# Kernel tuning notes

Hardware: AMD Instinct MI355X
Metric: run time of the kernel (lower is better)

The kernel has to match this reference:

```python
import jax, jax.numpy as jnp
import numpy as np

N_NODES = 50000
N_EDGES = 800000
IN_DIM = 128
HID_DIM = 128


def gcn_conv(x, edge_index, W, b):
    # PyG GCNConv: out = D^{-1/2} (A + I) D^{-1/2} X W + b
    n = x.shape[0]
    loop = jnp.arange(n)
    src = jnp.concatenate([edge_index[0], loop])
    dst = jnp.concatenate([edge_index[1], loop])
    deg = jax.ops.segment_sum(jnp.ones_like(dst, dtype=x.dtype), dst, num_segments=n)
    dinv = jax.lax.rsqrt(jnp.maximum(deg, 1.0))  # deg >= 1 with self-loops
    norm = dinv[src] * dinv[dst]                 # [E+N]
    h = x @ W                                    # [N, out_dim] dense transform first (smaller msgs)
    msg = h[src] * norm[:, None]                 # gather + scale
    return jax.ops.segment_sum(msg, dst, num_segments=n) + b  # scatter-add


def gcn_backbone(x, edge_index, W0, b0, W1, b1):
    h = jax.nn.relu(gcn_conv(x, edge_index, W0, b0))
    return gcn_conv(h, edge_index, W1, b1)


def setup_inputs() -> dict:
    key = jax.random.key(0)
    ks = jax.random.split(key, 8)
    s_in = 1.0 / np.sqrt(IN_DIM)
    s_h = 1.0 / np.sqrt(HID_DIM)
    return {
        "x1": jax.random.normal(ks[0], (N_NODES, IN_DIM), dtype=jnp.float32),
        "edge_index1": jax.random.randint(ks[1], (2, N_EDGES), 0, N_NODES, dtype=jnp.int32),
        "x2": jax.random.normal(ks[2], (N_NODES, IN_DIM), dtype=jnp.float32),
        "edge_index2": jax.random.randint(ks[3], (2, N_EDGES), 0, N_NODES, dtype=jnp.int32),
        "W0": jax.random.normal(ks[4], (IN_DIM, HID_DIM), dtype=jnp.float32) * s_in,
        "b0": jnp.zeros((HID_DIM,), dtype=jnp.float32),
        "W1": jax.random.normal(ks[5], (HID_DIM, HID_DIM), dtype=jnp.float32) * s_h,
        "b1": jnp.zeros((HID_DIM,), dtype=jnp.float32),
    }


def reference(x1, edge_index1, x2, edge_index2, W0, b0, W1, b1):
    z1 = gcn_backbone(x1, edge_index1, W0, b0, W1, b1)
    z2 = gcn_backbone(x2, edge_index2, W0, b0, W1, b1)
    return (z1, z2)
```

## Files before the change

kernel.cpp:

```cpp
#include <hip/hip_runtime.h>

#define GN 50000
#define GE 800000
#define GD 128
#define CAP 64
#define NBIN 8
#define BINW 6250
#define NCHUNK 400

typedef unsigned short u16;
typedef unsigned int u32;
typedef short bf16x8 __attribute__((ext_vector_type(8)));
typedef float f32x4 __attribute__((ext_vector_type(4)));
typedef u16 u16x8 __attribute__((ext_vector_type(8)));
typedef u16 u16x4 __attribute__((ext_vector_type(4)));

__device__ inline float bf2f_lo(u32 u) {
  union { u32 i; float f; } v; v.i = u << 16; return v.f;
}
__device__ inline float bf2f_hi(u32 u) {
  union { u32 i; float f; } v; v.i = u & 0xffff0000u; return v.f;
}
__device__ inline u16 f2bf(float f) {
  union { float f; u32 i; } v; v.f = f;
  u32 r = v.i + 0x7fffu + ((v.i >> 16) & 1u);
  return (u16)(r >> 16);
}
__device__ inline float rlf(float v, int l) {
  return __int_as_float(__builtin_amdgcn_readlane(__float_as_int(v), l));
}

__global__ __launch_bounds__(256) void k_build(const int* __restrict__ src,
                                               const int* __restrict__ dst,
                                               int* __restrict__ cnt,
                                               u16* __restrict__ bucket) {
  int bin = blockIdx.x & (NBIN - 1);
  int chunk = blockIdx.x >> 3;
  int t0 = chunk * 256 + threadIdx.x;
  const int stride = NCHUNK * 256;
  for (int e = t0; e < GE; e += stride) {
    int d = __builtin_nontemporal_load(&dst[e]);
    int s = __builtin_nontemporal_load(&src[e]);
    if (d / BINW == bin) {
      int slot = atomicAdd(&cnt[d], 1);
      if (slot < CAP) bucket[d * CAP + slot] = (u16)s;
    }
  }
}

__global__ __launch_bounds__(256) void k_dinv(const int* __restrict__ cnt,
                                              float* __restrict__ dinv) {
  int i = blockIdx.x * 256 + threadIdx.x;
  if (i >= GN) return;
  dinv[i] = rsqrtf((float)(cnt[i] + 1));
}

__global__ __launch_bounds__(256) void k_prep(const float* __restrict__ W0,
                                              const float* __restrict__ W1,
                                              u16* __restrict__ Wf0,
                                              u16* __restrict__ Wf1) {
  int idx = blockIdx.x * 256 + threadIdx.x;
  const float* W = (idx & 2048) ? W1 : W0;
  u16* Wf = (idx & 2048) ? Wf1 : Wf0;
  int r = idx & 2047;
  int kq = r >> 9, cb = (r >> 6) & 7, lane = r & 63;
  int m16 = lane & 15, quad = lane >> 4;
  int k0 = kq * 32 + quad * 8;
  int n = cb * 16 + m16;
  u16x8 o;
#pragma unroll
  for (int j = 0; j < 8; j++) o[j] = f2bf(W[(k0 + j) * 128 + n]);
  *(u16x8*)&Wf[((kq * 8 + cb) * 64 + lane) * 8] = o;
}

template <bool IN_F32>
__global__ __launch_bounds__(256, 4) void k_gemm(const void* __restrict__ Xin,
                                                 const u16* __restrict__ Wf,
                                                 u16* __restrict__ H) {
  __shared__ u16 Xs[64][136];
  int t = threadIdx.x;
  int lane = t & 63, wave = t >> 6;
  int m16 = lane & 15, quad = lane >> 4;
  int r0 = blockIdx.x * 64;

  bf16x8 bfr[4][2];
#pragma unroll
  for (int kq = 0; kq < 4; kq++)
#pragma unroll
    for (int c = 0; c < 2; c++)
      bfr[kq][c] = *(const bf16x8*)&Wf[((kq * 8 + wave * 2 + c) * 64 + lane) * 8];

  if (IN_F32) {
    const float4* Xv = (const float4*)Xin;
#pragma unroll
    for (int i = 0; i < 8; i++) {
      int idx = i * 256 + t;
      int row = idx >> 5, c4 = idx & 31;
      int gr = r0 + row; if (gr >= GN) gr = GN - 1;
      float4 v = Xv[(size_t)gr * 32 + c4];
      u16x4 u; u.x = f2bf(v.x); u.y = f2bf(v.y); u.z = f2bf(v.z); u.w = f2bf(v.w);
      *(u16x4*)&Xs[row][c4 * 4] = u;
    }
  } else {
    const u16x8* Xv = (const u16x8*)Xin;
#pragma unroll
    for (int i = 0; i < 4; i++) {
      int idx = i * 256 + t;
      int row = idx >> 4, c8 = idx & 15;
      int gr = r0 + row; if (gr >= GN) gr = GN - 1;
      *(u16x8*)&Xs[row][c8 * 8] = Xv[(size_t)gr * 16 + c8];
    }
  }
  __syncthreads();

  f32x4 acc[4][2] = {};
#pragma unroll
  for (int kq = 0; kq < 4; kq++) {
#pragma unroll
    for (int rb = 0; rb < 4; rb++) {
      bf16x8 a = *(const bf16x8*)&Xs[rb * 16 + m16][kq * 32 + quad * 8];
      acc[rb][0] = __builtin_amdgcn_mfma_f32_16x16x32_bf16(a, bfr[kq][0], acc[rb][0], 0, 0, 0);
      acc[rb][1] = __builtin_amdgcn_mfma_f32_16x16x32_bf16(a, bfr[kq][1], acc[rb][1], 0, 0, 0);
    }
  }

#pragma unroll
  for (int rb = 0; rb < 4; rb++) {
#pragma unroll
    for (int i = 0; i < 4; i++) {
      int grow = r0 + rb * 16 + quad * 4 + i;
      if (grow < GN) {
#pragma unroll
        for (int c = 0; c < 2; c++)
          H[(size_t)grow * 128 + (wave * 2 + c) * 16 + m16] = f2bf(acc[rb][c][i]);
      }
    }
  }
}

template <bool FINAL>
__global__ __launch_bounds__(256) void k_agg(const u16* __restrict__ H,
                                             const u16* __restrict__ bucket,
                                             const int* __restrict__ cnt,
                                             const float* __restrict__ dinv,
                                             const float* __restrict__ bias,
                                             void* __restrict__ out) {
  int wid = (blockIdx.x * 256 + threadIdx.x) >> 6;
  int lane = threadIdx.x & 63;
  if (wid >= GN) return;

  float dv = dinv[wid];
  int deg = min(cnt[wid], CAP);

  int s_l = 0;
  float d_l = 0.f;
  if (lane < deg) {
    s_l = (int)bucket[wid * CAP + lane];
    d_l = dinv[s_l];
  }

  const u32* Hv = (const u32*)H;
  u32 hs = Hv[(size_t)wid * 64 + lane];
  float ax = dv * bf2f_lo(hs);
  float ay = dv * bf2f_hi(hs);
  float2 bb = ((const float2*)bias)[lane];

  int dpad = (deg + 15) & ~15;
  for (int i = 0; i < dpad; i += 16) {
    int ss[16];
    u32 hh[16];
    float ww[16];
#pragma unroll
    for (int j = 0; j < 16; j++) ss[j] = __builtin_amdgcn_readlane(s_l, i + j);
#pragma unroll
    for (int j = 0; j < 16; j++) hh[j] = Hv[(size_t)ss[j] * 64 + lane];
#pragma unroll
    for (int j = 0; j < 16; j++) ww[j] = rlf(d_l, i + j);
#pragma unroll
    for (int j = 0; j < 16; j++) {
      ax += ww[j] * bf2f_lo(hh[j]);
      ay += ww[j] * bf2f_hi(hh[j]);
    }
  }

  float ox = dv * ax + bb.x;
  float oy = dv * ay + bb.y;
  if (!FINAL) {
    ox = fmaxf(ox, 0.f); oy = fmaxf(oy, 0.f);
    u32 packed = ((u32)f2bf(oy) << 16) | (u32)f2bf(ox);
    ((u32*)out)[(size_t)wid * 64 + lane] = packed;
  } else {
    ((float2*)out)[(size_t)wid * 64 + lane] = make_float2(ox, oy);
  }
}

extern "C" void kernel_launch(void* const* d_in, const int* in_sizes, int n_in,
                              void* d_out, int out_size, void* d_ws, size_t ws_size,
                              hipStream_t stream) {
  const float* x1 = (const float*)d_in[0];
  const int* ei1  = (const int*)d_in[1];
  const float* x2 = (const float*)d_in[2];
  const int* ei2  = (const int*)d_in[3];
  const float* W0 = (const float*)d_in[4];
  const float* b0 = (const float*)d_in[5];
  const float* W1 = (const float*)d_in[6];
  const float* b1 = (const float*)d_in[7];
  float* out = (float*)d_out;

  char* ws = (char*)d_ws;
  size_t off = 0;
  auto carve = [&](size_t bytes) -> char* {
    char* p = ws + off;
    off = (off + bytes + 511) & ~(size_t)511;
    return p;
  };
  int* cnt    = (int*)carve((size_t)GN * 4);
  float* dinv = (float*)carve((size_t)GN * 4);
  u16* bucket = (u16*)carve((size_t)GN * CAP * 2);
  u16* h      = (u16*)carve((size_t)GN * GD * 2);
  u16* a      = (u16*)carve((size_t)GN * GD * 2);
  u16* W0f    = (u16*)carve((size_t)GD * GD * 2);
  u16* W1f    = (u16*)carve((size_t)GD * GD * 2);

  k_prep<<<16, 256, 0, stream>>>(W0, W1, W0f, W1f);

  for (int g = 0; g < 2; g++) {
    const float* x = g ? x2 : x1;
    const int* src = g ? ei2 : ei1;
    const int* dst = src + GE;
    float* z = out + (size_t)g * GN * GD;

    hipMemsetAsync(cnt, 0, (size_t)GN * 4, stream);
    k_build<<<NBIN * NCHUNK, 256, 0, stream>>>(src, dst, cnt, bucket);
    k_dinv<<<(GN + 255) / 256, 256, 0, stream>>>(cnt, dinv);

    k_gemm<true><<<(GN + 63) / 64, 256, 0, stream>>>(x, W0f, h);
    k_agg<false><<<(GN * 64 + 255) / 256, 256, 0, stream>>>(h, bucket, cnt, dinv, b0, a);

    k_gemm<false><<<(GN + 63) / 64, 256, 0, stream>>>(a, W1f, h);
    k_agg<true><<<(GN * 64 + 255) / 256, 256, 0, stream>>>(h, bucket, cnt, dinv, b1, z);
  }
}
```

Measured before the change: 361.7 us.

## Batch both graphs into single launches and unroll edge loads in build

Processes both graphs in one launch per stage instead of looping over them. Every buffer (counts, dinv, buckets, hidden activations) is doubled, and kernels pick graph-specific pointers from the block or wave index. The goal is to halve the number of kernel launches and memsets and give each launch twice the parallelism, which helps fill the GPU during the small stages. k_build also issues all eight edge loads up front before doing the atomics, to add memory-level parallelism. The cost is twice the workspace and a larger cache footprint per launch.

```diff
diff --git a/kernel.cpp b/kernel.cpp
--- a/kernel.cpp
+++ b/kernel.cpp
@@ -30,20 +30,39 @@
   return __int_as_float(__builtin_amdgcn_readlane(__float_as_int(v), l));
 }
 
-__global__ __launch_bounds__(256) void k_build(const int* __restrict__ src,
-                                               const int* __restrict__ dst,
+__global__ __launch_bounds__(256) void k_build(const int* __restrict__ e1,
+                                               const int* __restrict__ e2,
                                                int* __restrict__ cnt,
                                                u16* __restrict__ bucket) {
-  int bin = blockIdx.x & (NBIN - 1);
-  int chunk = blockIdx.x >> 3;
+  const int half = NBIN * NCHUNK;
+  int gb = blockIdx.x >= half;
+  int bid = blockIdx.x - gb * half;
+  const int* E = gb ? e2 : e1;
+  const int* src = E;
+  const int* dst = E + GE;
+  int* c = cnt + gb * GN;
+  u16* bk = bucket + (size_t)gb * GN * CAP;
+
+  int bin = bid & (NBIN - 1);
+  int chunk = bid >> 3;
   int t0 = chunk * 256 + threadIdx.x;
   const int stride = NCHUNK * 256;
-  for (int e = t0; e < GE; e += stride) {
-    int d = __builtin_nontemporal_load(&dst[e]);
-    int s = __builtin_nontemporal_load(&src[e]);
-    if (d / BINW == bin) {
-      int slot = atomicAdd(&cnt[d], 1);
-      if (slot < CAP) bucket[d * CAP + slot] = (u16)s;
+  int lo = bin * BINW, hi = lo + BINW;
+
+  int s[8], d[8];
+#pragma unroll
+  for (int k = 0; k < 8; k++) {
+    int e = t0 + k * stride;
+    int ec = (e < GE) ? e : 0;
+    s[k] = __builtin_nontemporal_load(&src[ec]);
+    d[k] = __builtin_nontemporal_load(&dst[ec]);
+    if (e >= GE) d[k] = -1;
+  }
+#pragma unroll
+  for (int k = 0; k < 8; k++) {
+    if (d[k] >= lo && d[k] < hi) {
+      int slot = atomicAdd(&c[d[k]], 1);
+      if (slot < CAP) bk[d[k] * CAP + slot] = (u16)s[k];
     }
   }
 }
@@ -51,7 +70,7 @@
 __global__ __launch_bounds__(256) void k_dinv(const int* __restrict__ cnt,
                                               float* __restrict__ dinv) {
   int i = blockIdx.x * 256 + threadIdx.x;
-  if (i >= GN) return;
+  if (i >= 2 * GN) return;
   dinv[i] = rsqrtf((float)(cnt[i] + 1));
 }
 
@@ -73,15 +92,22 @@
   *(u16x8*)&Wf[((kq * 8 + cb) * 64 + lane) * 8] = o;
 }
 
+#define NB ((GN + 63) / 64)
 template <bool IN_F32>
-__global__ __launch_bounds__(256, 4) void k_gemm(const void* __restrict__ Xin,
+__global__ __launch_bounds__(256, 4) void k_gemm(const void* __restrict__ X1,
+                                                 const void* __restrict__ X2,
                                                  const u16* __restrict__ Wf,
                                                  u16* __restrict__ H) {
   __shared__ u16 Xs[64][136];
+  int gb = blockIdx.x >= NB;
+  int bid = blockIdx.x - gb * NB;
+  const void* Xin = gb ? X2 : X1;
+  u16* Hh = H + (size_t)gb * GN * GD;
+
   int t = threadIdx.x;
   int lane = t & 63, wave = t >> 6;
   int m16 = lane & 15, quad = lane >> 4;
-  int r0 = blockIdx.x * 64;
+  int r0 = bid * 64;
 
   bf16x8 bfr[4][2];
 #pragma unroll
@@ -132,7 +158,7 @@
       if (grow < GN) {
 #pragma unroll
         for (int c = 0; c < 2; c++)
-          H[(size_t)grow * 128 + (wave * 2 + c) * 16 + m16] = f2bf(acc[rb][c][i]);
+          Hh[(size_t)grow * 128 + (wave * 2 + c) * 16 + m16] = f2bf(acc[rb][c][i]);
       }
     }
   }
@@ -145,21 +171,27 @@
                                              const float* __restrict__ dinv,
                                              const float* __restrict__ bias,
                                              void* __restrict__ out) {
-  int wid = (blockIdx.x * 256 + threadIdx.x) >> 6;
+  int widg = (blockIdx.x * 256 + threadIdx.x) >> 6;
   int lane = threadIdx.x & 63;
-  if (wid >= GN) return;
-
-  float dv = dinv[wid];
-  int deg = min(cnt[wid], CAP);
+  if (widg >= 2 * GN) return;
+  int gb = widg >= GN;
+  int wid = widg - gb * GN;
+
+  const int* c = cnt + gb * GN;
+  const float* dvp = dinv + gb * GN;
+  const u16* bk = bucket + (size_t)gb * GN * CAP;
+  const u32* Hv = (const u32*)H + (size_t)gb * GN * 64;
+
+  float dv = dvp[wid];
+  int deg = min(c[wid], CAP);
 
   int s_l = 0;
   float d_l = 0.f;
   if (lane < deg) {
-    s_l = (int)bucket[wid * CAP + lane];
-    d_l = dinv[s_l];
-  }
-
-  const u32* Hv = (const u32*)H;
+    s_l = (int)bk[wid * CAP + lane];
+    d_l = dvp[s_l];
+  }
+
   u32 hs = Hv[(size_t)wid * 64 + lane];
   float ax = dv * bf2f_lo(hs);
   float ay = dv * bf2f_hi(hs);
@@ -188,9 +220,9 @@
   if (!FINAL) {
     ox = fmaxf(ox, 0.f); oy = fmaxf(oy, 0.f);
     u32 packed = ((u32)f2bf(oy) << 16) | (u32)f2bf(ox);
-    ((u32*)out)[(size_t)wid * 64 + lane] = packed;
+    ((u32*)out)[(size_t)widg * 64 + lane] = packed;
   } else {
-    ((float2*)out)[(size_t)wid * 64 + lane] = make_float2(ox, oy);
+    ((float2*)out)[(size_t)widg * 64 + lane] = make_float2(ox, oy);
   }
 }
 
@@ -214,30 +246,22 @@
     off = (off + bytes + 511) & ~(size_t)511;
     return p;
   };
-  int* cnt    = (int*)carve((size_t)GN * 4);
-  float* dinv = (float*)carve((size_t)GN * 4);
-  u16* bucket = (u16*)carve((size_t)GN * CAP * 2);
-  u16* h      = (u16*)carve((size_t)GN * GD * 2);
-  u16* a      = (u16*)carve((size_t)GN * GD * 2);
+  int* cnt    = (int*)carve((size_t)2 * GN * 4);
+  float* dinv = (float*)carve((size_t)2 * GN * 4);
+  u16* bucket = (u16*)carve((size_t)2 * GN * CAP * 2);
+  u16* h      = (u16*)carve((size_t)2 * GN * GD * 2);
+  u16* a      = (u16*)carve((size_t)2 * GN * GD * 2);
   u16* W0f    = (u16*)carve((size_t)GD * GD * 2);
   u16* W1f    = (u16*)carve((size_t)GD * GD * 2);
 
   k_prep<<<16, 256, 0, stream>>>(W0, W1, W0f, W1f);
-
-  for (int g = 0; g < 2; g++) {
-    const float* x = g ? x2 : x1;
-    const int* src = g ? ei2 : ei1;
-    const int* dst = src + GE;
-    float* z = out + (size_t)g * GN * GD;
-
-    hipMemsetAsync(cnt, 0, (size_t)GN * 4, stream);
-    k_build<<<NBIN * NCHUNK, 256, 0, stream>>>(src, dst, cnt, bucket);
-    k_dinv<<<(GN + 255) / 256, 256, 0, stream>>>(cnt, dinv);
-
-    k_gemm<true><<<(GN + 63) / 64, 256, 0, stream>>>(x, W0f, h);
-    k_agg<false><<<(GN * 64 + 255) / 256, 256, 0, stream>>>(h, bucket, cnt, dinv, b0, a);
-
-    k_gemm<false><<<(GN + 63) / 64, 256, 0, stream>>>(a, W1f, h);
-    k_agg<true><<<(GN * 64 + 255) / 256, 256, 0, stream>>>(h, bucket, cnt, dinv, b1, z);
-  }
-}
+  hipMemsetAsync(cnt, 0, (size_t)2 * GN * 4, stream);
+  k_build<<<2 * NBIN * NCHUNK, 256, 0, stream>>>(ei1, ei2, cnt, bucket);
+  k_dinv<<<(2 * GN + 255) / 256, 256, 0, stream>>>(cnt, dinv);
+
+  k_gemm<true><<<2 * NB, 256, 0, stream>>>(x1, x2, W0f, h);
+  k_agg<false><<<(2 * GN * 64 + 255) / 256, 256, 0, stream>>>(h, bucket, cnt, dinv, b0, a);
+
+  k_gemm<false><<<2 * NB, 256, 0, stream>>>(a, a + (size_t)GN * GD, W1f, h);
+  k_agg<true><<<(2 * GN * 64 + 255) / 256, 256, 0, stream>>>(h, bucket, cnt, dinv, b1, out);
+}
```

Result: faster. 327.0 us (-9.6%).
